# Kernel tuning notes

Hardware: AMD Instinct MI355X
Metric: run time of the kernel (lower is better)

## Reference

```python
import jax, jax.numpy as jnp
from jax import lax
import numpy as np

B, T, F, H, L = 256, 512, 16, 256, 2


def _lstm_layer(x, w_ih, w_hh, b_ih, b_hh):
    # x: [B, T, in]; w_ih: [4H, in]; w_hh: [4H, H]; biases: [4H]
    # PyTorch gate order: i, f, g, o
    x_proj = jnp.einsum('bti,gi->btg', x, w_ih) + b_ih + b_hh  # [B, T, 4H]
    h0 = jnp.zeros((x.shape[0], w_hh.shape[1]), x.dtype)
    c0 = h0

    def step(carry, xp):
        h, c = carry
        gates = xp + h @ w_hh.T  # [B, 4H]
        i, f, g, o = jnp.split(gates, 4, axis=-1)
        c = jax.nn.sigmoid(f) * c + jax.nn.sigmoid(i) * jnp.tanh(g)
        h = jax.nn.sigmoid(o) * jnp.tanh(c)
        return (h, c), h

    _, hs = lax.scan(step, (h0, c0), jnp.swapaxes(x_proj, 0, 1))  # [T, B, H]
    return jnp.swapaxes(hs, 0, 1)  # [B, T, H]


def setup_inputs() -> dict:
    key = jax.random.key(0)
    ks = jax.random.split(key, 16)
    x = jax.random.normal(ks[0], (B, T, F), dtype=jnp.float32)
    lengths = jax.random.randint(ks[1], (B,), 1, T + 1)  # in [1, T]
    s = 1.0 / np.sqrt(H)
    u = lambda k, shape: jax.random.uniform(k, shape, jnp.float32, -s, s)
    inp = {'x': x, 'lengths': lengths}
    in_dims = [F, H]
    for l in range(L):
        inp[f'w_ih{l}'] = u(ks[2 + 4 * l], (4 * H, in_dims[l]))
        inp[f'w_hh{l}'] = u(ks[3 + 4 * l], (4 * H, H))
        inp[f'b_ih{l}'] = u(ks[4 + 4 * l], (4 * H,))
        inp[f'b_hh{l}'] = u(ks[5 + 4 * l], (4 * H,))
    inp['fc_w'] = u(ks[10], (1, H))
    inp['fc_b'] = u(ks[11], (1,))
    return inp


def reference(x, lengths, w_ih0, w_hh0, b_ih0, b_hh0,
              w_ih1, w_hh1, b_ih1, b_hh1, fc_w, fc_b):
    # Packed LSTM: outputs at t >= length never influence last_outputs
    # (recurrence only flows forward in time), so running the dense
    # full-length LSTM and gathering at lengths-1 is mathematically identical.
    h = _lstm_layer(x, w_ih0, w_hh0, b_ih0, b_hh0)
    h = _lstm_layer(h, w_ih1, w_hh1, b_ih1, b_hh1)
    last = h[jnp.arange(h.shape[0]), lengths - 1]  # [B, H]
    return jax.nn.relu(last) @ fc_w.T + fc_b  # [B, 1]
```

## Files before the change

### kernel.cpp

```cpp
#include <hip/hip_runtime.h>
#include <hip/hip_fp16.h>


#define Tc 32
#define NCHUNK 16

#define OFF_IH0   0
#define OFF_B0    16384
#define OFF_B1    17408
#define OFF_C0S   18432
#define OFF_C1S   84480
#define OFF_H1S   150528
#define OFF_HLAST 216576
#define FP_END    282624
#define H_HH0  0
#define H_HH1  262144
#define H_IH1  524288
#define H_H0C  786432
#define H0SLOT 2113536
#define H_XP1  5013504
#define XPSLOT 8454144

#define SMEM_BYTES 66560

typedef _Float16 v2h __attribute__((ext_vector_type(2)));

__device__ __forceinline__ unsigned packh2(float a, float b) {
  __half2 h = __floats2half2_rn(a, b);
  return *(unsigned*)&h;
}
__device__ __forceinline__ float4 dot4(const float4 w, const v2h h, float4 acc) {
  const v2h* wg = (const v2h*)&w;
  acc.x = __builtin_amdgcn_fdot2(wg[0], h, acc.x, false);
  acc.y = __builtin_amdgcn_fdot2(wg[1], h, acc.y, false);
  acc.z = __builtin_amdgcn_fdot2(wg[2], h, acc.z, false);
  acc.w = __builtin_amdgcn_fdot2(wg[3], h, acc.w, false);
  return acc;
}
__device__ __forceinline__ float sigf(float x) {
  return __fdividef(1.f, 1.f + __expf(-x));
}
__device__ __forceinline__ float tanhf_fast(float x) {
  float ax = fabsf(x);
  float e = __expf(-2.f * ax);
  float t = __fdividef(1.f - e, 1.f + e);
  return copysignf(t, x);
}
__device__ __forceinline__ float h2f(unsigned short s) {
  __half h = __builtin_bit_cast(__half, s);
  return __half2float(h);
}
__device__ __forceinline__ float4 cvt4(ushort4 v) {
  float4 r;
  r.x = h2f(v.x); r.y = h2f(v.y); r.z = h2f(v.z); r.w = h2f(v.w);
  return r;
}
__device__ __forceinline__ v2h u2h(unsigned v) {
  return __builtin_bit_cast(v2h, v);
}
__device__ __forceinline__ void lds_barrier() {
  asm volatile("s_waitcnt lgkmcnt(0)" ::: "memory");
  __builtin_amdgcn_s_barrier();
  __builtin_amdgcn_sched_barrier(0);
}

__global__ __launch_bounds__(256) void prep_kernel(
    const float* __restrict__ w_ih0, const float* __restrict__ w_hh0,
    const float* __restrict__ b_ih0, const float* __restrict__ b_hh0,
    const float* __restrict__ w_ih1, const float* __restrict__ w_hh1,
    const float* __restrict__ b_ih1, const float* __restrict__ b_hh1,
    float* __restrict__ ws) {
  const int idx = blockIdx.x * blockDim.x + threadIdx.x;
  const int g = idx & 3, u = (idx >> 2) & 255, p = idx >> 10;
  const int j = g * 256 + u;
  unsigned* h16u = (unsigned*)(ws + FP_END);
  h16u[H_HH0 / 2 + idx] = packh2(w_hh0[j * 256 + 2 * p], w_hh0[j * 256 + 2 * p + 1]);
  h16u[H_HH1 / 2 + idx] = packh2(w_hh1[j * 256 + 2 * p], w_hh1[j * 256 + 2 * p + 1]);
  h16u[H_IH1 / 2 + idx] = packh2(w_ih1[j * 256 + 2 * p], w_ih1[j * 256 + 2 * p + 1]);
  if (idx < 8192) {
    ((unsigned*)(ws + OFF_IH0))[idx] =
        packh2(w_ih0[j * 16 + 2 * p], w_ih0[j * 16 + 2 * p + 1]);
  }
  if (idx < 1024) {
    ws[OFF_B0 + idx] = b_ih0[j] + b_hh0[j];
    ws[OFF_B1 + idx] = b_ih1[j] + b_hh1[j];
  }
}

__global__ __launch_bounds__(512)
__attribute__((amdgpu_waves_per_eu(2, 2)))
void fused_kernel(
    float* __restrict__ ws, const float* __restrict__ x,
    const int* __restrict__ lengths, int step) {
  extern __shared__ __align__(16) char smem_raw[];
  const int bid = blockIdx.x;
  const int tid = threadIdx.x;
  __half* h16 = (__half*)(ws + FP_END);
  unsigned short* h0cS = (unsigned short*)(h16 + H_H0C);
  unsigned short* xpS = (unsigned short*)(h16 + H_XP1);

  if (bid < 86) {
    if (step >= NCHUNK) return;
    const int kc = step;
    const int kh = tid >> 8, u = tid & 255;
    const int bg = bid * 3;
    unsigned short* hb = (unsigned short*)smem_raw;
    unsigned* xsp = (unsigned*)(smem_raw + 4096);
    float* scratch = (float*)(smem_raw + 4352);
    float4* wxl = (float4*)(smem_raw + 18048);

    int len[3];
    #pragma unroll
    for (int b = 0; b < 3; ++b) len[b] = (bg + b < 256) ? lengths[bg + b] : 1;
    const int tmaxb = max(len[0], max(len[1], len[2]));
    if (kc * Tc >= tmaxb) return;
    const int tend = min(Tc, tmaxb - kc * Tc);
    const int slot = kc & 1, slotP = slot ^ 1;

    {
      const float4* gwx = (const float4*)(ws + OFF_IH0);
      #pragma unroll
      for (int e = 0; e < 4; ++e) wxl[tid + e * 512] = gwx[tid + e * 512];
    }

    const float4* wqR = (const float4*)(h16 + H_HH0) + (size_t)(kh * 64) * 256 + u;
    float4 wreg[32];
    #pragma unroll
    for (int p = 0; p < 32; ++p) wreg[p] = wqR[p * 256];
    const float4* wqS = wqR + 32 * 256;
    const float4 bias = ((const float4*)(ws + OFF_B0))[u];

    float c[3] = {0.f, 0.f, 0.f};
    if (kh == 0) {
      #pragma unroll
      for (int b = 0; b < 3; ++b) {
        unsigned short hv = 0;
        if (kc > 0) {
          hv = h0cS[(size_t)slotP * H0SLOT + ((size_t)(bg + b) * 32 + 31) * 256 + u];
          c[b] = ws[OFF_C0S + (bg + b) * 256 + u];
        }
        hb[0 * 768 + b * 256 + u] = hv;
      }
    }
    if (tid < 24) {
      int b = tid >> 3, i = tid & 7;
      int bb = min(bg + b, 255);
      const float* xp = x + (size_t)bb * 8192 + (kc * Tc) * 16;
      xsp[0 * 24 + b * 8 + i] = packh2(xp[2 * i], xp[2 * i + 1]);
    }
    __syncthreads();

    for (int tc = 0; tc < tend; ++tc) {
      const int cur = tc & 1, nxt = cur ^ 1;
      float4 A0, A1, A2;
      if (kh == 0) { A0 = bias; A1 = bias; A2 = bias; }
      else { A0 = make_float4(0, 0, 0, 0); A1 = A0; A2 = A0; }

      #pragma unroll
      for (int p = 0; p < 4; ++p) {
        float4 w = wxl[(kh * 4 + p) * 256 + u];
        v2h x0 = u2h(xsp[cur * 24 + 0 * 8 + kh * 4 + p]);
        v2h x1 = u2h(xsp[cur * 24 + 1 * 8 + kh * 4 + p]);
        v2h x2 = u2h(xsp[cur * 24 + 2 * 8 + kh * 4 + p]);
        A0 = dot4(w, x0, A0);
        A1 = dot4(w, x1, A1);
        A2 = dot4(w, x2, A2);
      }

      const float4* h0r0 = (const float4*)(hb + cur * 768 + 0 * 256 + kh * 128);
      const float4* h0r1 = (const float4*)(hb + cur * 768 + 1 * 256 + kh * 128);
      const float4* h0r2 = (const float4*)(hb + cur * 768 + 2 * 256 + kh * 128);

      #pragma unroll
      for (int grp = 0; grp < 8; ++grp) {
        float4 h40 = h0r0[grp], h41 = h0r1[grp], h42 = h0r2[grp];
        const v2h* hp0 = (const v2h*)&h40;
        const v2h* hp1 = (const v2h*)&h41;
        const v2h* hp2 = (const v2h*)&h42;
        #pragma unroll
        for (int q = 0; q < 4; ++q) {
          A0 = dot4(wreg[grp * 4 + q], hp0[q], A0);
          A1 = dot4(wreg[grp * 4 + q], hp1[q], A1);
          A2 = dot4(wreg[grp * 4 + q], hp2[q], A2);
        }
      }
      {
        float4 B[3][4];
        #pragma unroll
        for (int p = 0; p < 4; ++p) {
          B[0][p] = wqS[p * 256];
          B[1][p] = wqS[(4 + p) * 256];
        }
        #pragma unroll
        for (int g = 0; g < 8; ++g) {
          if (g + 2 < 8) {
            #pragma unroll
            for (int p = 0; p < 4; ++p)
              B[(g + 2) % 3][p] = wqS[((g + 2) * 4 + p) * 256];
          }
          const float4* wbuf = B[g % 3];
          float4 h40 = h0r0[8 + g], h41 = h0r1[8 + g], h42 = h0r2[8 + g];
          const v2h* hp0 = (const v2h*)&h40;
          const v2h* hp1 = (const v2h*)&h41;
          const v2h* hp2 = (const v2h*)&h42;
          #pragma unroll
          for (int q = 0; q < 4; ++q) {
            A0 = dot4(wbuf[q], hp0[q], A0);
            A1 = dot4(wbuf[q], hp1[q], A1);
            A2 = dot4(wbuf[q], hp2[q], A2);
          }
        }
      }

      if (kh == 1) {
        #pragma unroll
        for (int g = 0; g < 4; ++g) {
          scratch[u * 13 + g] = ((const float*)&A0)[g];
          scratch[u * 13 + 4 + g] = ((const float*)&A1)[g];
          scratch[u * 13 + 8 + g] = ((const float*)&A2)[g];
        }
        if (tid < 256 + 24) {
          int bi = tid - 256, b = bi >> 3, i = bi & 7;
          int bb = min(bg + b, 255);
          int tn = min(kc * Tc + tc + 1, 511);
          const float* xp = x + (size_t)bb * 8192 + tn * 16;
          xsp[nxt * 24 + b * 8 + i] = packh2(xp[2 * i], xp[2 * i + 1]);
        }
      }
      lds_barrier();
      if (kh == 0) {
        float4 B0, B1, B2;
        #pragma unroll
        for (int g = 0; g < 4; ++g) {
          ((float*)&B0)[g] = scratch[u * 13 + g];
          ((float*)&B1)[g] = scratch[u * 13 + 4 + g];
          ((float*)&B2)[g] = scratch[u * 13 + 8 + g];
        }
        A0.x += B0.x; A0.y += B0.y; A0.z += B0.z; A0.w += B0.w;
        A1.x += B1.x; A1.y += B1.y; A1.z += B1.z; A1.w += B1.w;
        A2.x += B2.x; A2.y += B2.y; A2.z += B2.z; A2.w += B2.w;
        float4 A[3] = {A0, A1, A2};
        #pragma unroll
        for (int b = 0; b < 3; ++b) {
          float ig = sigf(A[b].x), fg = sigf(A[b].y);
          float gg = tanhf_fast(A[b].z), og = sigf(A[b].w);
          c[b] = fg * c[b] + ig * gg;
          float h = og * tanhf_fast(c[b]);
          unsigned short hu = __half_as_ushort(__float2half(h));
          hb[nxt * 768 + b * 256 + u] = hu;
          h0cS[(size_t)slot * H0SLOT + ((size_t)(bg + b) * 32 + tc) * 256 + u] = hu;
        }
      }
      lds_barrier();
    }
    if (kh == 0) {
      #pragma unroll
      for (int b = 0; b < 3; ++b) ws[OFF_C0S + (bg + b) * 256 + u] = c[b];
    }

  } else if (bid < 172) {
    if (step < 2 || step >= NCHUNK + 2) return;
    const int kc = step - 2;
    const int kh = tid >> 8, u = tid & 255;
    const int bg = (bid - 86) * 3;
    unsigned short* h1b = (unsigned short*)smem_raw;
    float* scratch = (float*)(smem_raw + 4096);

    int len[3];
    #pragma unroll
    for (int b = 0; b < 3; ++b) len[b] = (bg + b < 256) ? lengths[bg + b] : 1;
    const int tmaxb = max(len[0], max(len[1], len[2]));
    if (kc * Tc >= tmaxb) return;
    const int tend = min(Tc, tmaxb - kc * Tc);
    const int slot = kc & 1;

    const float4* wqR = (const float4*)(h16 + H_HH1) + (size_t)(kh * 64) * 256 + u;
    float4 wreg[32];
    #pragma unroll
    for (int p = 0; p < 32; ++p) wreg[p] = wqR[p * 256];
    const float4* wqS = wqR + 32 * 256;

    float c[3] = {0.f, 0.f, 0.f}, hout[3] = {0.f, 0.f, 0.f};
    if (kh == 0) {
      #pragma unroll
      for (int b = 0; b < 3; ++b) {
        float hv = 0.f;
        if (kc > 0) {
          hv = ws[OFF_H1S + (bg + b) * 256 + u];
          c[b] = ws[OFF_C1S + (bg + b) * 256 + u];
        }
        h1b[0 * 768 + b * 256 + u] = __half_as_ushort(__float2half(hv));
      }
    }
    const unsigned short* xb =
        xpS + (size_t)slot * XPSLOT + (size_t)bg * 32768 + u * 4;
    ushort4 xc0, xc1, xc2;
    if (kh == 0) {
      xc0 = *(const ushort4*)(xb);
      xc1 = *(const ushort4*)(xb + 32768);
      xc2 = *(const ushort4*)(xb + 65536);
    }
    __syncthreads();

    for (int tc = 0; tc < tend; ++tc) {
      const int cur = tc & 1, nxt = cur ^ 1;
      float4 A0, A1, A2;
      ushort4 xn0, xn1, xn2;
      if (kh == 0) {
        A0 = cvt4(xc0); A1 = cvt4(xc1); A2 = cvt4(xc2);
        if (tc + 1 < tend) {
          xn0 = *(const ushort4*)(xb + (tc + 1) * 1024);
          xn1 = *(const ushort4*)(xb + 32768 + (tc + 1) * 1024);
          xn2 = *(const ushort4*)(xb + 65536 + (tc + 1) * 1024);
        }
      } else { A0 = make_float4(0, 0, 0, 0); A1 = A0; A2 = A0; }

      const float4* r0 = (const float4*)(h1b + cur * 768 + 0 * 256 + kh * 128);
      const float4* r1 = (const float4*)(h1b + cur * 768 + 1 * 256 + kh * 128);
      const float4* r2 = (const float4*)(h1b + cur * 768 + 2 * 256 + kh * 128);

      #pragma unroll
      for (int grp = 0; grp < 8; ++grp) {
        float4 h40 = r0[grp], h41 = r1[grp], h42 = r2[grp];
        const v2h* hp0 = (const v2h*)&h40;
        const v2h* hp1 = (const v2h*)&h41;
        const v2h* hp2 = (const v2h*)&h42;
        #pragma unroll
        for (int q = 0; q < 4; ++q) {
          A0 = dot4(wreg[grp * 4 + q], hp0[q], A0);
          A1 = dot4(wreg[grp * 4 + q], hp1[q], A1);
          A2 = dot4(wreg[grp * 4 + q], hp2[q], A2);
        }
      }
      {
        float4 B[3][4];
        #pragma unroll
        for (int p = 0; p < 4; ++p) {
          B[0][p] = wqS[p * 256];
          B[1][p] = wqS[(4 + p) * 256];
        }
        #pragma unroll
        for (int g = 0; g < 8; ++g) {
          if (g + 2 < 8) {
            #pragma unroll
            for (int p = 0; p < 4; ++p)
              B[(g + 2) % 3][p] = wqS[((g + 2) * 4 + p) * 256];
          }
          const float4* wbuf = B[g % 3];
          float4 h40 = r0[8 + g], h41 = r1[8 + g], h42 = r2[8 + g];
          const v2h* hp0 = (const v2h*)&h40;
          const v2h* hp1 = (const v2h*)&h41;
          const v2h* hp2 = (const v2h*)&h42;
          #pragma unroll
          for (int q = 0; q < 4; ++q) {
            A0 = dot4(wbuf[q], hp0[q], A0);
            A1 = dot4(wbuf[q], hp1[q], A1);
            A2 = dot4(wbuf[q], hp2[q], A2);
          }
        }
      }

      if (kh == 1) {
        #pragma unroll
        for (int g = 0; g < 4; ++g) {
          scratch[u * 13 + g] = ((const float*)&A0)[g];
          scratch[u * 13 + 4 + g] = ((const float*)&A1)[g];
          scratch[u * 13 + 8 + g] = ((const float*)&A2)[g];
        }
      }
      lds_barrier();
      if (kh == 0) {
        float4 B0, B1, B2;
        #pragma unroll
        for (int g = 0; g < 4; ++g) {
          ((float*)&B0)[g] = scratch[u * 13 + g];
          ((float*)&B1)[g] = scratch[u * 13 + 4 + g];
          ((float*)&B2)[g] = scratch[u * 13 + 8 + g];
        }
        A0.x += B0.x; A0.y += B0.y; A0.z += B0.z; A0.w += B0.w;
        A1.x += B1.x; A1.y += B1.y; A1.z += B1.z; A1.w += B1.w;
        A2.x += B2.x; A2.y += B2.y; A2.z += B2.z; A2.w += B2.w;
        float4 A[3] = {A0, A1, A2};
        const int t = kc * Tc + tc;
        #pragma unroll
        for (int b = 0; b < 3; ++b) {
          float ig = sigf(A[b].x), fg = sigf(A[b].y);
          float gg = tanhf_fast(A[b].z), og = sigf(A[b].w);
          c[b] = fg * c[b] + ig * gg;
          float h = og * tanhf_fast(c[b]);
          hout[b] = h;
          h1b[nxt * 768 + b * 256 + u] = __half_as_ushort(__float2half(h));
          if (t == len[b] - 1) ws[OFF_HLAST + (bg + b) * 256 + u] = h;
        }
        xc0 = xn0; xc1 = xn1; xc2 = xn2;
      }
      lds_barrier();
    }
    if (kh == 0) {
      #pragma unroll
      for (int b = 0; b < 3; ++b) {
        ws[OFF_C1S + (bg + b) * 256 + u] = c[b];
        ws[OFF_H1S + (bg + b) * 256 + u] = hout[b];
      }
    }

  } else {
    if (step < 1 || step >= NCHUNK + 1) return;
    if (bid >= 236) return;
    const int kc = step - 1;
    const int gid = bid - 172;
    const int b0g = gid * 4;
    const int rt = tid & 63, wv = tid >> 6;
    __half2* hc2 = (__half2*)smem_raw;

    int lmax = 0;
    #pragma unroll
    for (int i = 0; i < 4; ++i) lmax = max(lmax, lengths[b0g + i]);
    if (kc * Tc >= lmax) return;
    const int slot = kc & 1;

    {
      const unsigned short* src =
          h0cS + (size_t)slot * H0SLOT + (size_t)b0g * 8192;
      const int cl = tid & 127, pg = tid >> 7;
      #pragma unroll
      for (int pp = 0; pp < 32; pp += 4) {
        const int p0 = pg * 32 + pp;
        uint4 v = *(const uint4*)(src + (size_t)cl * 256 + p0 * 2);
        unsigned* d = (unsigned*)hc2;
        d[(p0 + 0) * 128 + cl] = v.x;
        d[(p0 + 1) * 128 + cl] = v.y;
        d[(p0 + 2) * 128 + cl] = v.z;
        d[(p0 + 3) * 128 + cl] = v.w;
      }
    }
    __syncthreads();

    const __half* Wb = h16 + H_IH1;
    unsigned short* xdst = xpS + (size_t)slot * XPSLOT;
    #pragma unroll 1
    for (int rp = 0; rp < 2; ++rp) {
      #pragma unroll 1
      for (int cp = 0; cp < 2; ++cp) {
        const int uA = rp * 128 + rt, uB = uA + 64;
        const int c0 = cp * 64 + wv * 8;
        const float4 bA = ((const float4*)(ws + OFF_B1))[uA];
        const float4 bB = ((const float4*)(ws + OFF_B1))[uB];
        float accA[4][8], accB[4][8];
        #pragma unroll
        for (int g = 0; g < 4; ++g)
          #pragma unroll
          for (int cc = 0; cc < 8; ++cc) {
            accA[g][cc] = ((const float*)&bA)[g];
            accB[g][cc] = ((const float*)&bB)[g];
          }
        #pragma unroll 2
        for (int p = 0; p < 128; ++p) {
          float4 wA = *(const float4*)(Wb + (size_t)p * 2048 + uA * 8);
          float4 wB = *(const float4*)(Wb + (size_t)p * 2048 + uB * 8);
          float4 h0v = *(const float4*)(hc2 + p * 128 + c0);
          float4 h1v = *(const float4*)(hc2 + p * 128 + c0 + 4);
          const v2h* ga = (const v2h*)&wA;
          const v2h* gb = (const v2h*)&wB;
          const v2h* hv = (const v2h*)&h0v;
          const v2h* hw = (const v2h*)&h1v;
          #pragma unroll
          for (int g = 0; g < 4; ++g) {
            #pragma unroll
            for (int cc = 0; cc < 4; ++cc) {
              accA[g][cc] = __builtin_amdgcn_fdot2(ga[g], hv[cc], accA[g][cc], false);
              accA[g][cc + 4] = __builtin_amdgcn_fdot2(ga[g], hw[cc], accA[g][cc + 4], false);
              accB[g][cc] = __builtin_amdgcn_fdot2(gb[g], hv[cc], accB[g][cc], false);
              accB[g][cc + 4] = __builtin_amdgcn_fdot2(gb[g], hw[cc], accB[g][cc + 4], false);
            }
          }
        }
        #pragma unroll
        for (int cc = 0; cc < 8; ++cc) {
          const int col = c0 + cc;
          const size_t cb = ((size_t)(b0g + (col >> 5)) * 32 + (col & 31)) * 1024;
          ushort4 oA, oB;
          oA.x = __half_as_ushort(__float2half(accA[0][cc]));
          oA.y = __half_as_ushort(__float2half(accA[1][cc]));
          oA.z = __half_as_ushort(__float2half(accA[2][cc]));
          oA.w = __half_as_ushort(__float2half(accA[3][cc]));
          oB.x = __half_as_ushort(__float2half(accB[0][cc]));
          oB.y = __half_as_ushort(__float2half(accB[1][cc]));
          oB.z = __half_as_ushort(__float2half(accB[2][cc]));
          oB.w = __half_as_ushort(__float2half(accB[3][cc]));
          *(ushort4*)(xdst + cb + uA * 4) = oA;
          *(ushort4*)(xdst + cb + uB * 4) = oB;
        }
      }
    }
  }
}

__global__ __launch_bounds__(256) void fc_kernel(
    const float* __restrict__ ws, const float* __restrict__ fc_w,
    const float* __restrict__ fc_b, float* __restrict__ out) {
  __shared__ float red[256];
  const int tid = threadIdx.x;
  const int b = blockIdx.x;
  red[tid] = fmaxf(ws[OFF_HLAST + b * 256 + tid], 0.f) * fc_w[tid];
  __syncthreads();
  #pragma unroll
  for (int s = 128; s > 0; s >>= 1) {
    if (tid < s) red[tid] += red[tid + s];
    __syncthreads();
  }
  if (tid == 0) out[b] = red[0] + fc_b[0];
}

extern "C" void kernel_launch(void* const* d_in, const int* in_sizes, int n_in,
                              void* d_out, int out_size, void* d_ws, size_t ws_size,
                              hipStream_t stream) {
  const float* x     = (const float*)d_in[0];
  const int*   lens  = (const int*)d_in[1];
  const float* w_ih0 = (const float*)d_in[2];
  const float* w_hh0 = (const float*)d_in[3];
  const float* b_ih0 = (const float*)d_in[4];
  const float* b_hh0 = (const float*)d_in[5];
  const float* w_ih1 = (const float*)d_in[6];
  const float* w_hh1 = (const float*)d_in[7];
  const float* b_ih1 = (const float*)d_in[8];
  const float* b_hh1 = (const float*)d_in[9];
  const float* fc_w  = (const float*)d_in[10];
  const float* fc_b  = (const float*)d_in[11];
  float* out = (float*)d_out;
  float* ws  = (float*)d_ws;

  hipLaunchKernelGGL(prep_kernel, dim3(512), dim3(256), 0, stream,
                     w_ih0, w_hh0, b_ih0, b_hh0, w_ih1, w_hh1, b_ih1, b_hh1, ws);
  hipFuncSetAttribute(reinterpret_cast<const void*>(fused_kernel),
                      hipFuncAttributeMaxDynamicSharedMemorySize, SMEM_BYTES);
  for (int k = 0; k < NCHUNK + 2; ++k) {
    hipLaunchKernelGGL(fused_kernel, dim3(236), dim3(512), SMEM_BYTES, stream,
                       ws, x, lens, k);
  }
  hipLaunchKernelGGL(fc_kernel, dim3(256), dim3(256), 0, stream,
                     ws, fc_w, fc_b, out);
}
```

Before: 3.100 ms.

## Split recurrent matvec K-dimension four ways across 1024-thread blocks

```diff
diff --git a/kernel.cpp b/kernel.cpp
--- a/kernel.cpp
+++ b/kernel.cpp
@@ -21,7 +21,7 @@
 #define H_XP1  5013504
 #define XPSLOT 8454144
 
-#define SMEM_BYTES 66560
+#define SMEM_BYTES 76032
 
 typedef _Float16 v2h __attribute__((ext_vector_type(2)));
 
@@ -87,9 +87,7 @@
   }
 }
 
-__global__ __launch_bounds__(512)
-__attribute__((amdgpu_waves_per_eu(2, 2)))
-void fused_kernel(
+__global__ __launch_bounds__(1024) void fused_kernel(
     float* __restrict__ ws, const float* __restrict__ x,
     const int* __restrict__ lengths, int step) {
   extern __shared__ __align__(16) char smem_raw[];
@@ -102,12 +100,12 @@
   if (bid < 86) {
     if (step >= NCHUNK) return;
     const int kc = step;
-    const int kh = tid >> 8, u = tid & 255;
+    const int kh4 = tid >> 8, u = tid & 255;
     const int bg = bid * 3;
     unsigned short* hb = (unsigned short*)smem_raw;
-    unsigned* xsp = (unsigned*)(smem_raw + 4096);
-    float* scratch = (float*)(smem_raw + 4352);
-    float4* wxl = (float4*)(smem_raw + 18048);
+    unsigned* xsp = (unsigned*)(smem_raw + 3072);
+    float* scratch = (float*)(smem_raw + 3264);
+    float4* wxl = (float4*)(smem_raw + 43200);
 
     int len[3];
     #pragma unroll
@@ -119,19 +117,14 @@
 
     {
       const float4* gwx = (const float4*)(ws + OFF_IH0);
-      #pragma unroll
-      for (int e = 0; e < 4; ++e) wxl[tid + e * 512] = gwx[tid + e * 512];
-    }
-
-    const float4* wqR = (const float4*)(h16 + H_HH0) + (size_t)(kh * 64) * 256 + u;
-    float4 wreg[32];
-    #pragma unroll
-    for (int p = 0; p < 32; ++p) wreg[p] = wqR[p * 256];
-    const float4* wqS = wqR + 32 * 256;
+      wxl[tid] = gwx[tid];
+      wxl[tid + 1024] = gwx[tid + 1024];
+    }
     const float4 bias = ((const float4*)(ws + OFF_B0))[u];
+    const float4* wq = (const float4*)(h16 + H_HH0) + (size_t)(kh4 * 32) * 256 + u;
 
     float c[3] = {0.f, 0.f, 0.f};
-    if (kh == 0) {
+    if (kh4 == 0) {
       #pragma unroll
       for (int b = 0; b < 3; ++b) {
         unsigned short hv = 0;
@@ -153,53 +146,39 @@
     for (int tc = 0; tc < tend; ++tc) {
       const int cur = tc & 1, nxt = cur ^ 1;
       float4 A0, A1, A2;
-      if (kh == 0) { A0 = bias; A1 = bias; A2 = bias; }
+      if (kh4 == 0) { A0 = bias; A1 = bias; A2 = bias; }
       else { A0 = make_float4(0, 0, 0, 0); A1 = A0; A2 = A0; }
 
       #pragma unroll
-      for (int p = 0; p < 4; ++p) {
-        float4 w = wxl[(kh * 4 + p) * 256 + u];
-        v2h x0 = u2h(xsp[cur * 24 + 0 * 8 + kh * 4 + p]);
-        v2h x1 = u2h(xsp[cur * 24 + 1 * 8 + kh * 4 + p]);
-        v2h x2 = u2h(xsp[cur * 24 + 2 * 8 + kh * 4 + p]);
+      for (int p = 0; p < 2; ++p) {
+        float4 w = wxl[(kh4 * 2 + p) * 256 + u];
+        v2h x0 = u2h(xsp[cur * 24 + 0 * 8 + kh4 * 2 + p]);
+        v2h x1 = u2h(xsp[cur * 24 + 1 * 8 + kh4 * 2 + p]);
+        v2h x2 = u2h(xsp[cur * 24 + 2 * 8 + kh4 * 2 + p]);
         A0 = dot4(w, x0, A0);
         A1 = dot4(w, x1, A1);
         A2 = dot4(w, x2, A2);
       }
 
-      const float4* h0r0 = (const float4*)(hb + cur * 768 + 0 * 256 + kh * 128);
-      const float4* h0r1 = (const float4*)(hb + cur * 768 + 1 * 256 + kh * 128);
-      const float4* h0r2 = (const float4*)(hb + cur * 768 + 2 * 256 + kh * 128);
-
-      #pragma unroll
-      for (int grp = 0; grp < 8; ++grp) {
-        float4 h40 = h0r0[grp], h41 = h0r1[grp], h42 = h0r2[grp];
-        const v2h* hp0 = (const v2h*)&h40;
-        const v2h* hp1 = (const v2h*)&h41;
-        const v2h* hp2 = (const v2h*)&h42;
-        #pragma unroll
-        for (int q = 0; q < 4; ++q) {
-          A0 = dot4(wreg[grp * 4 + q], hp0[q], A0);
-          A1 = dot4(wreg[grp * 4 + q], hp1[q], A1);
-          A2 = dot4(wreg[grp * 4 + q], hp2[q], A2);
-        }
-      }
+      const unsigned short* hbc = hb + cur * 768;
       {
-        float4 B[3][4];
+        float4 Bf[3][4];
         #pragma unroll
         for (int p = 0; p < 4; ++p) {
-          B[0][p] = wqS[p * 256];
-          B[1][p] = wqS[(4 + p) * 256];
+          Bf[0][p] = wq[p * 256];
+          Bf[1][p] = wq[(4 + p) * 256];
         }
         #pragma unroll
         for (int g = 0; g < 8; ++g) {
           if (g + 2 < 8) {
             #pragma unroll
             for (int p = 0; p < 4; ++p)
-              B[(g + 2) % 3][p] = wqS[((g + 2) * 4 + p) * 256];
+              Bf[(g + 2) % 3][p] = wq[((g + 2) * 4 + p) * 256];
           }
-          const float4* wbuf = B[g % 3];
-          float4 h40 = h0r0[8 + g], h41 = h0r1[8 + g], h42 = h0r2[8 + g];
+          const float4* wbuf = Bf[g % 3];
+          float4 h40 = *(const float4*)(hbc + 0 * 256 + kh4 * 64 + g * 8);
+          float4 h41 = *(const float4*)(hbc + 1 * 256 + kh4 * 64 + g * 8);
+          float4 h42 = *(const float4*)(hbc + 2 * 256 + kh4 * 64 + g * 8);
           const v2h* hp0 = (const v2h*)&h40;
           const v2h* hp1 = (const v2h*)&h41;
           const v2h* hp2 = (const v2h*)&h42;
@@ -212,33 +191,28 @@
         }
       }
 
-      if (kh == 1) {
-        #pragma unroll
-        for (int g = 0; g < 4; ++g) {
-          scratch[u * 13 + g] = ((const float*)&A0)[g];
-          scratch[u * 13 + 4 + g] = ((const float*)&A1)[g];
-          scratch[u * 13 + 8 + g] = ((const float*)&A2)[g];
-        }
-        if (tid < 256 + 24) {
-          int bi = tid - 256, b = bi >> 3, i = bi & 7;
-          int bb = min(bg + b, 255);
-          int tn = min(kc * Tc + tc + 1, 511);
-          const float* xp = x + (size_t)bb * 8192 + tn * 16;
-          xsp[nxt * 24 + b * 8 + i] = packh2(xp[2 * i], xp[2 * i + 1]);
-        }
+      if (kh4 > 0) {
+        float* sc = scratch + (kh4 - 1) * 3328 + u * 13;
+        sc[0] = A0.x; sc[1] = A0.y; sc[2] = A0.z; sc[3] = A0.w;
+        sc[4] = A1.x; sc[5] = A1.y; sc[6] = A1.z; sc[7] = A1.w;
+        sc[8] = A2.x; sc[9] = A2.y; sc[10] = A2.z; sc[11] = A2.w;
+      }
+      if (tid >= 768 && tid < 792) {
+        int bi = tid - 768, b = bi >> 3, i = bi & 7;
+        int bb = min(bg + b, 255);
+        int tn = min(kc * Tc + tc + 1, 511);
+        const float* xp = x + (size_t)bb * 8192 + tn * 16;
+        xsp[nxt * 24 + b * 8 + i] = packh2(xp[2 * i], xp[2 * i + 1]);
       }
       lds_barrier();
-      if (kh == 0) {
-        float4 B0, B1, B2;
-        #pragma unroll
-        for (int g = 0; g < 4; ++g) {
-          ((float*)&B0)[g] = scratch[u * 13 + g];
-          ((float*)&B1)[g] = scratch[u * 13 + 4 + g];
-          ((float*)&B2)[g] = scratch[u * 13 + 8 + g];
-        }
-        A0.x += B0.x; A0.y += B0.y; A0.z += B0.z; A0.w += B0.w;
-        A1.x += B1.x; A1.y += B1.y; A1.z += B1.z; A1.w += B1.w;
-        A2.x += B2.x; A2.y += B2.y; A2.z += B2.z; A2.w += B2.w;
+      if (kh4 == 0) {
+        #pragma unroll
+        for (int r = 0; r < 3; ++r) {
+          const float* so = scratch + r * 3328 + u * 13;
+          A0.x += so[0]; A0.y += so[1]; A0.z += so[2]; A0.w += so[3];
+          A1.x += so[4]; A1.y += so[5]; A1.z += so[6]; A1.w += so[7];
+          A2.x += so[8]; A2.y += so[9]; A2.z += so[10]; A2.w += so[11];
+        }
         float4 A[3] = {A0, A1, A2};
         #pragma unroll
         for (int b = 0; b < 3; ++b) {
@@ -253,7 +227,7 @@
       }
       lds_barrier();
     }
-    if (kh == 0) {
+    if (kh4 == 0) {
       #pragma unroll
       for (int b = 0; b < 3; ++b) ws[OFF_C0S + (bg + b) * 256 + u] = c[b];
     }
@@ -261,10 +235,10 @@
   } else if (bid < 172) {
     if (step < 2 || step >= NCHUNK + 2) return;
     const int kc = step - 2;
-    const int kh = tid >> 8, u = tid & 255;
+    const int kh4 = tid >> 8, u = tid & 255;
     const int bg = (bid - 86) * 3;
     unsigned short* h1b = (unsigned short*)smem_raw;
-    float* scratch = (float*)(smem_raw + 4096);
+    float* scratch = (float*)(smem_raw + 3264);
 
     int len[3];
     #pragma unroll
@@ -274,14 +248,10 @@
     const int tend = min(Tc, tmaxb - kc * Tc);
     const int slot = kc & 1;
 
-    const float4* wqR = (const float4*)(h16 + H_HH1) + (size_t)(kh * 64) * 256 + u;
-    float4 wreg[32];
-    #pragma unroll
-    for (int p = 0; p < 32; ++p) wreg[p] = wqR[p * 256];
-    const float4* wqS = wqR + 32 * 256;
+    const float4* wq = (const float4*)(h16 + H_HH1) + (size_t)(kh4 * 32) * 256 + u;
 
     float c[3] = {0.f, 0.f, 0.f}, hout[3] = {0.f, 0.f, 0.f};
-    if (kh == 0) {
+    if (kh4 == 0) {
       #pragma unroll
       for (int b = 0; b < 3; ++b) {
         float hv = 0.f;
@@ -295,7 +265,7 @@
     const unsigned short* xb =
         xpS + (size_t)slot * XPSLOT + (size_t)bg * 32768 + u * 4;
     ushort4 xc0, xc1, xc2;
-    if (kh == 0) {
+    if (kh4 == 0) {
       xc0 = *(const ushort4*)(xb);
       xc1 = *(const ushort4*)(xb + 32768);
       xc2 = *(const ushort4*)(xb + 65536);
@@ -306,7 +276,7 @@
       const int cur = tc & 1, nxt = cur ^ 1;
       float4 A0, A1, A2;
       ushort4 xn0, xn1, xn2;
-      if (kh == 0) {
+      if (kh4 == 0) {
         A0 = cvt4(xc0); A1 = cvt4(xc1); A2 = cvt4(xc2);
         if (tc + 1 < tend) {
           xn0 = *(const ushort4*)(xb + (tc + 1) * 1024);
@@ -315,39 +285,25 @@
         }
       } else { A0 = make_float4(0, 0, 0, 0); A1 = A0; A2 = A0; }
 
-      const float4* r0 = (const float4*)(h1b + cur * 768 + 0 * 256 + kh * 128);
-      const float4* r1 = (const float4*)(h1b + cur * 768 + 1 * 256 + kh * 128);
-      const float4* r2 = (const float4*)(h1b + cur * 768 + 2 * 256 + kh * 128);
-
-      #pragma unroll
-      for (int grp = 0; grp < 8; ++grp) {
-        float4 h40 = r0[grp], h41 = r1[grp], h42 = r2[grp];
-        const v2h* hp0 = (const v2h*)&h40;
-        const v2h* hp1 = (const v2h*)&h41;
-        const v2h* hp2 = (const v2h*)&h42;
-        #pragma unroll
-        for (int q = 0; q < 4; ++q) {
-          A0 = dot4(wreg[grp * 4 + q], hp0[q], A0);
-          A1 = dot4(wreg[grp * 4 + q], hp1[q], A1);
-          A2 = dot4(wreg[grp * 4 + q], hp2[q], A2);
-        }
-      }
+      const unsigned short* hbc = h1b + cur * 768;
       {
-        float4 B[3][4];
+        float4 Bf[3][4];
         #pragma unroll
         for (int p = 0; p < 4; ++p) {
-          B[0][p] = wqS[p * 256];
-          B[1][p] = wqS[(4 + p) * 256];
+          Bf[0][p] = wq[p * 256];
+          Bf[1][p] = wq[(4 + p) * 256];
         }
         #pragma unroll
         for (int g = 0; g < 8; ++g) {
           if (g + 2 < 8) {
             #pragma unroll
             for (int p = 0; p < 4; ++p)
-              B[(g + 2) % 3][p] = wqS[((g + 2) * 4 + p) * 256];
+              Bf[(g + 2) % 3][p] = wq[((g + 2) * 4 + p) * 256];
           }
-          const float4* wbuf = B[g % 3];
-          float4 h40 = r0[8 + g], h41 = r1[8 + g], h42 = r2[8 + g];
+          const float4* wbuf = Bf[g % 3];
+          float4 h40 = *(const float4*)(hbc + 0 * 256 + kh4 * 64 + g * 8);
+          float4 h41 = *(const float4*)(hbc + 1 * 256 + kh4 * 64 + g * 8);
+          float4 h42 = *(const float4*)(hbc + 2 * 256 + kh4 * 64 + g * 8);
           const v2h* hp0 = (const v2h*)&h40;
           const v2h* hp1 = (const v2h*)&h41;
           const v2h* hp2 = (const v2h*)&h42;
@@ -360,26 +316,21 @@
         }
       }
 
-      if (kh == 1) {
-        #pragma unroll
-        for (int g = 0; g < 4; ++g) {
-          scratch[u * 13 + g] = ((const float*)&A0)[g];
-          scratch[u * 13 + 4 + g] = ((const float*)&A1)[g];
-          scratch[u * 13 + 8 + g] = ((const float*)&A2)[g];
-        }
+      if (kh4 > 0) {
+        float* sc = scratch + (kh4 - 1) * 3328 + u * 13;
+        sc[0] = A0.x; sc[1] = A0.y; sc[2] = A0.z; sc[3] = A0.w;
+        sc[4] = A1.x; sc[5] = A1.y; sc[6] = A1.z; sc[7] = A1.w;
+        sc[8] = A2.x; sc[9] = A2.y; sc[10] = A2.z; sc[11] = A2.w;
       }
       lds_barrier();
-      if (kh == 0) {
-        float4 B0, B1, B2;
-        #pragma unroll
-        for (int g = 0; g < 4; ++g) {
-          ((float*)&B0)[g] = scratch[u * 13 + g];
-          ((float*)&B1)[g] = scratch[u * 13 + 4 + g];
-          ((float*)&B2)[g] = scratch[u * 13 + 8 + g];
-        }
-        A0.x += B0.x; A0.y += B0.y; A0.z += B0.z; A0.w += B0.w;
-        A1.x += B1.x; A1.y += B1.y; A1.z += B1.z; A1.w += B1.w;
-        A2.x += B2.x; A2.y += B2.y; A2.z += B2.z; A2.w += B2.w;
+      if (kh4 == 0) {
+        #pragma unroll
+        for (int r = 0; r < 3; ++r) {
+          const float* so = scratch + r * 3328 + u * 13;
+          A0.x += so[0]; A0.y += so[1]; A0.z += so[2]; A0.w += so[3];
+          A1.x += so[4]; A1.y += so[5]; A1.z += so[6]; A1.w += so[7];
+          A2.x += so[8]; A2.y += so[9]; A2.z += so[10]; A2.w += so[11];
+        }
         float4 A[3] = {A0, A1, A2};
         const int t = kc * Tc + tc;
         #pragma unroll
@@ -396,7 +347,7 @@
       }
       lds_barrier();
     }
-    if (kh == 0) {
+    if (kh4 == 0) {
       #pragma unroll
       for (int b = 0; b < 3; ++b) {
         ws[OFF_C1S + (bg + b) * 256 + u] = c[b];
@@ -410,7 +361,9 @@
     const int kc = step - 1;
     const int gid = bid - 172;
     const int b0g = gid * 4;
-    const int rt = tid & 63, wv = tid >> 6;
+    const int rt = tid & 63;
+    const int wv16 = tid >> 6;
+    const int rp = wv16 >> 3, wv = wv16 & 7;
     __half2* hc2 = (__half2*)smem_raw;
 
     int lmax = 0;
@@ -424,8 +377,8 @@
           h0cS + (size_t)slot * H0SLOT + (size_t)b0g * 8192;
       const int cl = tid & 127, pg = tid >> 7;
       #pragma unroll
-      for (int pp = 0; pp < 32; pp += 4) {
-        const int p0 = pg * 32 + pp;
+      for (int pp = 0; pp < 16; pp += 4) {
+        const int p0 = pg * 16 + pp;
         uint4 v = *(const uint4*)(src + (size_t)cl * 256 + p0 * 2);
         unsigned* d = (unsigned*)hc2;
         d[(p0 + 0) * 128 + cl] = v.x;
@@ -439,58 +392,55 @@
     const __half* Wb = h16 + H_IH1;
     unsigned short* xdst = xpS + (size_t)slot * XPSLOT;
     #pragma unroll 1
-    for (int rp = 0; rp < 2; ++rp) {
-      #pragma unroll 1
-      for (int cp = 0; cp < 2; ++cp) {
-        const int uA = rp * 128 + rt, uB = uA + 64;
-        const int c0 = cp * 64 + wv * 8;
-        const float4 bA = ((const float4*)(ws + OFF_B1))[uA];
-        const float4 bB = ((const float4*)(ws + OFF_B1))[uB];
-        float accA[4][8], accB[4][8];
-        #pragma unroll
-        for (int g = 0; g < 4; ++g)
+    for (int cp = 0; cp < 2; ++cp) {
+      const int uA = rp * 128 + rt, uB = uA + 64;
+      const int c0 = cp * 64 + wv * 8;
+      const float4 bA = ((const float4*)(ws + OFF_B1))[uA];
+      const float4 bB = ((const float4*)(ws + OFF_B1))[uB];
+      float accA[4][8], accB[4][8];
+      #pragma unroll
+      for (int g = 0; g < 4; ++g)
+        #pragma unroll
+        for (int cc = 0; cc < 8; ++cc) {
+          accA[g][cc] = ((const float*)&bA)[g];
+          accB[g][cc] = ((const float*)&bB)[g];
+        }
+      #pragma unroll 2
+      for (int p = 0; p < 128; ++p) {
+        float4 wA = *(const float4*)(Wb + (size_t)p * 2048 + uA * 8);
+        float4 wB = *(const float4*)(Wb + (size_t)p * 2048 + uB * 8);
+        float4 h0v = *(const float4*)(hc2 + p * 128 + c0);
+        float4 h1v = *(const float4*)(hc2 + p * 128 + c0 + 4);
+        const v2h* ga = (const v2h*)&wA;
+        const v2h* gb = (const v2h*)&wB;
+        const v2h* hv = (const v2h*)&h0v;
+        const v2h* hw = (const v2h*)&h1v;
+        #pragma unroll
+        for (int g = 0; g < 4; ++g) {
           #pragma unroll
-          for (int cc = 0; cc < 8; ++cc) {
-            accA[g][cc] = ((const float*)&bA)[g];
-            accB[g][cc] = ((const float*)&bB)[g];
+          for (int cc = 0; cc < 4; ++cc) {
+            accA[g][cc] = __builtin_amdgcn_fdot2(ga[g], hv[cc], accA[g][cc], false);
+            accA[g][cc + 4] = __builtin_amdgcn_fdot2(ga[g], hw[cc], accA[g][cc + 4], false);
+            accB[g][cc] = __builtin_amdgcn_fdot2(gb[g], hv[cc], accB[g][cc], false);
+            accB[g][cc + 4] = __builtin_amdgcn_fdot2(gb[g], hw[cc], accB[g][cc + 4], false);
           }
-        #pragma unroll 2
-        for (int p = 0; p < 128; ++p) {
-          float4 wA = *(const float4*)(Wb + (size_t)p * 2048 + uA * 8);
-          float4 wB = *(const float4*)(Wb + (size_t)p * 2048 + uB * 8);
-          float4 h0v = *(const float4*)(hc2 + p * 128 + c0);
-          float4 h1v = *(const float4*)(hc2 + p * 128 + c0 + 4);
-          const v2h* ga = (const v2h*)&wA;
-          const v2h* gb = (const v2h*)&wB;
-          const v2h* hv = (const v2h*)&h0v;
-          const v2h* hw = (const v2h*)&h1v;
-          #pragma unroll
-          for (int g = 0; g < 4; ++g) {
-            #pragma unroll
-            for (int cc = 0; cc < 4; ++cc) {
-              accA[g][cc] = __builtin_amdgcn_fdot2(ga[g], hv[cc], accA[g][cc], false);
-              accA[g][cc + 4] = __builtin_amdgcn_fdot2(ga[g], hw[cc], accA[g][cc + 4], false);
-              accB[g][cc] = __builtin_amdgcn_fdot2(gb[g], hv[cc], accB[g][cc], false);
-              accB[g][cc + 4] = __builtin_amdgcn_fdot2(gb[g], hw[cc], accB[g][cc + 4], false);
-            }
-          }
-        }
-        #pragma unroll
-        for (int cc = 0; cc < 8; ++cc) {
-          const int col = c0 + cc;
-          const size_t cb = ((size_t)(b0g + (col >> 5)) * 32 + (col & 31)) * 1024;
-          ushort4 oA, oB;
-          oA.x = __half_as_ushort(__float2half(accA[0][cc]));
-          oA.y = __half_as_ushort(__float2half(accA[1][cc]));
-          oA.z = __half_as_ushort(__float2half(accA[2][cc]));
-          oA.w = __half_as_ushort(__float2half(accA[3][cc]));
-          oB.x = __half_as_ushort(__float2half(accB[0][cc]));
-          oB.y = __half_as_ushort(__float2half(accB[1][cc]));
-          oB.z = __half_as_ushort(__float2half(accB[2][cc]));
-          oB.w = __half_as_ushort(__float2half(accB[3][cc]));
-          *(ushort4*)(xdst + cb + uA * 4) = oA;
-          *(ushort4*)(xdst + cb + uB * 4) = oB;
-        }
+        }
+      }
+      #pragma unroll
+      for (int cc = 0; cc < 8; ++cc) {
+        const int col = c0 + cc;
+        const size_t cb = ((size_t)(b0g + (col >> 5)) * 32 + (col & 31)) * 1024;
+        ushort4 oA, oB;
+        oA.x = __half_as_ushort(__float2half(accA[0][cc]));
+        oA.y = __half_as_ushort(__float2half(accA[1][cc]));
+        oA.z = __half_as_ushort(__float2half(accA[2][cc]));
+        oA.w = __half_as_ushort(__float2half(accA[3][cc]));
+        oB.x = __half_as_ushort(__float2half(accB[0][cc]));
+        oB.y = __half_as_ushort(__float2half(accB[1][cc]));
+        oB.z = __half_as_ushort(__float2half(accB[2][cc]));
+        oB.w = __half_as_ushort(__float2half(accB[3][cc]));
+        *(ushort4*)(xdst + cb + uA * 4) = oA;
+        *(ushort4*)(xdst + cb + uB * 4) = oB;
       }
     }
   }
@@ -535,7 +485,7 @@
   hipFuncSetAttribute(reinterpret_cast<const void*>(fused_kernel),
                       hipFuncAttributeMaxDynamicSharedMemorySize, SMEM_BYTES);
   for (int k = 0; k < NCHUNK + 2; ++k) {
-    hipLaunchKernelGGL(fused_kernel, dim3(236), dim3(512), SMEM_BYTES, stream,
+    hipLaunchKernelGGL(fused_kernel, dim3(236), dim3(1024), SMEM_BYTES, stream,
                        ws, x, lens, k);
   }
   hipLaunchKernelGGL(fc_kernel, dim3(256), dim3(256), 0, stream,
```

After: 3.931 ms. 1.27x slower.
